# Kernel optimization log

Hardware: AMD Instinct MI355X
Metric: run time of the kernel (lower is better)

The kernel has to match this reference:

```python
import jax, jax.numpy as jnp
import numpy as np

TABLE_NUM = 16
TABLE_SIZE_LOG2 = 12
T = 1 << TABLE_SIZE_LOG2          # 4096 entries per table
FEAT = 2                          # features per entry (mini_linear in = table_num*2)
Z_DIM = 512
RES_MIN = 16
RES_MAX = 256
IMG = 256
MLP_HIDDEN = 64
OUT_DIM = 3
BATCH = 8
PRIME_Y = np.uint32(2654435761)   # instant-NGP spatial hash prime


def setup_inputs() -> dict:
    key = jax.random.key(0)
    ks = jax.random.split(key, 9)
    d_tab = TABLE_NUM * T * FEAT
    return {
        "z": jax.random.normal(ks[0], (BATCH, Z_DIM), jnp.float32),
        "w_table": jax.random.normal(ks[1], (Z_DIM, d_tab), jnp.float32) * 1e-2,
        "b_table": jnp.zeros((d_tab,), jnp.float32),
        "w1": jax.random.normal(ks[2], (TABLE_NUM * FEAT, MLP_HIDDEN), jnp.float32) * (1.0 / np.sqrt(TABLE_NUM * FEAT)),
        "b1": jnp.zeros((MLP_HIDDEN,), jnp.float32),
        "w2": jax.random.normal(ks[3], (MLP_HIDDEN, MLP_HIDDEN), jnp.float32) * (1.0 / np.sqrt(MLP_HIDDEN)),
        "b2": jnp.zeros((MLP_HIDDEN,), jnp.float32),
        "w3": jax.random.normal(ks[4], (MLP_HIDDEN, OUT_DIM), jnp.float32) * (1.0 / np.sqrt(MLP_HIDDEN)),
        "b3": jnp.zeros((OUT_DIM,), jnp.float32),
    }


def _sample_coords(b):
    c = (jnp.arange(IMG, dtype=jnp.float32) + 0.5) / IMG
    xx, yy = jnp.meshgrid(c, c, indexing="ij")  # torch.meshgrid default
    coords = jnp.stack([xx, yy], axis=-1).reshape(1, -1, 2)
    return jnp.broadcast_to(coords, (b, IMG * IMG, 2))


def _hash_retrieve(tables, coords):
    """tables: B x L x T x F; coords: B x N x 2 in [0,1). Returns B x N x (L*F)."""
    B, L, _, _ = tables.shape
    growth = np.exp((np.log(RES_MAX) - np.log(RES_MIN)) / (L - 1))
    offs = jnp.array([[0, 0], [1, 0], [0, 1], [1, 1]], dtype=jnp.uint32)  # 4 corners
    bidx = jnp.arange(B)[:, None, None]
    feats = []
    for l in range(L):
        res = jnp.float32(RES_MIN * (growth ** l))
        pos = coords * res                      # B,N,2
        pos0 = jnp.floor(pos)
        frac = pos - pos0                       # B,N,2
        corner = pos0.astype(jnp.uint32)[:, :, None, :] + offs[None, None]  # B,N,4,2
        idx = (corner[..., 0] ^ (corner[..., 1] * PRIME_Y)) & jnp.uint32(T - 1)
        f = tables[:, l][bidx, idx.astype(jnp.int32)]        # B,N,4,F gather
        fx, fy = frac[..., 0], frac[..., 1]
        w = jnp.stack([(1 - fx) * (1 - fy), fx * (1 - fy),
                       (1 - fx) * fy,       fx * fy], axis=-1)  # B,N,4
        feats.append(jnp.einsum("bncf,bnc->bnf", f, w))
    return jnp.concatenate(feats, axis=-1)


def reference(z, w_table, b_table, w1, b1, w2, b2, w3, b3):
    B = z.shape[0]
    tables = (z @ w_table + b_table).reshape(B, TABLE_NUM, T, FEAT)
    coords = _sample_coords(B).astype(tables.dtype)
    feat = _hash_retrieve(tables, coords)                    # B,N,L*F
    h = jax.nn.relu(feat @ w1 + b1)
    h = jax.nn.relu(h @ w2 + b2)
    o = jnp.tanh(h @ w3 + b3)                                # B,N,3
    return o.reshape(B, IMG, IMG, OUT_DIM).transpose(0, 3, 1, 2)
```

## Files before the change

kernel.cpp:

```cpp
#include <hip/hip_runtime.h>
#include <cmath>

#define TABLE_NUM 16
#define T_SIZE    4096
#define Z_DIM     512
#define IMG       256
#define D_TAB     (TABLE_NUM * T_SIZE * 2)
#define BATCH     8
#define HID       64
#define N_PIX     (IMG * IMG)
#define PRIME_Y   2654435761u
#define KCHUNK    4
#define KLEN      (Z_DIM / KCHUNK)
#define NG4       (D_TAB / 4)

typedef _Float16 v8h  __attribute__((ext_vector_type(8)));
typedef _Float16 v2h  __attribute__((ext_vector_type(2)));
typedef float    v4f  __attribute__((ext_vector_type(4)));

struct ResArr { float r[TABLE_NUM]; };

__global__ void prep_weights(const float* __restrict__ w1, const float* __restrict__ w2,
                             const float* __restrict__ w3, const float* __restrict__ z,
                             _Float16* __restrict__ w1T, _Float16* __restrict__ w2T,
                             _Float16* __restrict__ w3T, float* __restrict__ zT)
{
    const int t0  = blockIdx.x * 256 + threadIdx.x;
    const int stp = gridDim.x * 256;
    for (int i = t0; i < HID * 32; i += stp) {
        int n = i >> 5, k = i & 31;
        w1T[i] = (_Float16)w1[k * HID + n];
    }
    for (int i = t0; i < HID * HID; i += stp) {
        int n = i >> 6, k = i & 63;
        w2T[i] = (_Float16)w2[k * HID + n];
    }
    for (int i = t0; i < 16 * HID; i += stp) {
        int n = i >> 6, k = i & 63;
        w3T[i] = (_Float16)(n < 3 ? w3[k * 3 + n] : 0.f);
    }
    for (int i = t0; i < Z_DIM * BATCH; i += stp) {
        int k = i >> 3, b = i & 7;
        zT[i] = z[b * Z_DIM + k];
    }
}

__global__ __launch_bounds__(256) void gen_partial(
    const float* __restrict__ zT, const float* __restrict__ w,
    float* __restrict__ part)
{
    const int c  = blockIdx.x >> 7;
    const int g  = (blockIdx.x & 127) * 256 + threadIdx.x;
    const int k0 = c * KLEN;
    const float4* wp = reinterpret_cast<const float4*>(w) + g;

    float4 acc[BATCH];
#pragma unroll
    for (int b = 0; b < BATCH; ++b) acc[b] = make_float4(0.f, 0.f, 0.f, 0.f);

#pragma unroll 8
    for (int kk = 0; kk < KLEN; ++kk) {
        const int k = k0 + kk;
        float4 wv = wp[(size_t)k * NG4];
        const float* zr = zT + k * BATCH;
#pragma unroll
        for (int b = 0; b < BATCH; ++b) {
            float zv = zr[b];
            acc[b].x = fmaf(zv, wv.x, acc[b].x);
            acc[b].y = fmaf(zv, wv.y, acc[b].y);
            acc[b].z = fmaf(zv, wv.z, acc[b].z);
            acc[b].w = fmaf(zv, wv.w, acc[b].w);
        }
    }

    float4* pp = reinterpret_cast<float4*>(part);
#pragma unroll
    for (int b = 0; b < BATCH; ++b)
        pp[((size_t)(c * BATCH + b) << 15) + g] = acc[b];
}

__global__ __launch_bounds__(256) void gen_reduce(
    const float* __restrict__ part, const float* __restrict__ bt,
    float* __restrict__ tabs)
{
    const int i = blockIdx.x * 256 + threadIdx.x;
    const int b = i >> 15, g = i & (NG4 - 1);
    const float4* pp = reinterpret_cast<const float4*>(part);

    float4 s = pp[((size_t)b << 15) + g];
#pragma unroll
    for (int c = 1; c < KCHUNK; ++c) {
        float4 p = pp[((size_t)(c * BATCH + b) << 15) + g];
        s.x += p.x; s.y += p.y; s.z += p.z; s.w += p.w;
    }
    float4 bv = reinterpret_cast<const float4*>(bt)[g];
    s.x += bv.x; s.y += bv.y; s.z += bv.z; s.w += bv.w;
    reinterpret_cast<float4*>(tabs)[((size_t)b << 15) + g] = s;
}

__global__ __launch_bounds__(256) void hash_mlp(
    const float* __restrict__ tabs,
    const _Float16* __restrict__ w1T, const _Float16* __restrict__ w2T,
    const _Float16* __restrict__ w3T,
    const float* __restrict__ b1, const float* __restrict__ b2,
    const float* __restrict__ b3,
    float* __restrict__ out, ResArr res)
{
    __shared__ _Float16 mbuf[4][64][72];
    const int tid  = threadIdx.x;
    const int wid  = tid >> 6;
    const int lane = tid & 63;
    const int b    = blockIdx.x & 7;
    const int tile = blockIdx.x >> 3;
    const int i0   = (tile >> 4) * 16 + wid * 4;
    const int j0   = (tile & 15) * 16;

    const int di = lane >> 4, dj = lane & 15;
    const float cx = ((float)(i0 + di) + 0.5f) * (1.0f / IMG);
    const float cy = ((float)(j0 + dj) + 0.5f) * (1.0f / IMG);
    const float2* tb2 = reinterpret_cast<const float2*>(tabs + (size_t)b * D_TAB);

#pragma unroll 4
    for (int l = 0; l < TABLE_NUM; ++l) {
        float r  = res.r[l];
        float px = cx * r, py = cy * r;
        float fx0 = floorf(px), fy0 = floorf(py);
        float fx = px - fx0, fy = py - fy0;
        unsigned x0 = (unsigned)(int)fx0, y0 = (unsigned)(int)fy0;
        unsigned hy0 = y0 * PRIME_Y, hy1 = (y0 + 1u) * PRIME_Y;
        unsigned i00 = (x0 ^ hy0) & (T_SIZE - 1);
        unsigned i10 = ((x0 + 1u) ^ hy0) & (T_SIZE - 1);
        unsigned i01 = (x0 ^ hy1) & (T_SIZE - 1);
        unsigned i11 = ((x0 + 1u) ^ hy1) & (T_SIZE - 1);
        const float2* tl = tb2 + l * T_SIZE;
        float2 f00 = tl[i00], f10 = tl[i10], f01 = tl[i01], f11 = tl[i11];
        float w00 = (1.f - fx) * (1.f - fy);
        float w10 = fx * (1.f - fy);
        float w01 = (1.f - fx) * fy;
        float w11 = fx * fy;
        float e0 = f00.x * w00 + f10.x * w10 + f01.x * w01 + f11.x * w11;
        float e1 = f00.y * w00 + f10.y * w10 + f01.y * w01 + f11.y * w11;
        v2h p; p.x = (_Float16)e0; p.y = (_Float16)e1;
        *reinterpret_cast<v2h*>(&mbuf[wid][lane][2 * l]) = p;
    }

    const int arow = lane & 15;
    const int kgrp = lane >> 4;

    v8h a1[4];
#pragma unroll
    for (int mt = 0; mt < 4; ++mt)
        a1[mt] = *reinterpret_cast<const v8h*>(&mbuf[wid][mt * 16 + arow][kgrp * 8]);

#pragma unroll
    for (int nt = 0; nt < 4; ++nt) {
        v8h bf1 = *reinterpret_cast<const v8h*>(&w1T[(nt * 16 + arow) * 32 + kgrp * 8]);
        const float bias = b1[nt * 16 + arow];
#pragma unroll
        for (int mt = 0; mt < 4; ++mt) {
            v4f c = {0.f, 0.f, 0.f, 0.f};
            c = __builtin_amdgcn_mfma_f32_16x16x32_f16(a1[mt], bf1, c, 0, 0, 0);
#pragma unroll
            for (int e = 0; e < 4; ++e)
                mbuf[wid][mt * 16 + kgrp * 4 + e][nt * 16 + arow] =
                    (_Float16)fmaxf(c[e] + bias, 0.f);
        }
    }

    v8h a2[4][2];
#pragma unroll
    for (int mt = 0; mt < 4; ++mt) {
        a2[mt][0] = *reinterpret_cast<const v8h*>(&mbuf[wid][mt * 16 + arow][kgrp * 8]);
        a2[mt][1] = *reinterpret_cast<const v8h*>(&mbuf[wid][mt * 16 + arow][32 + kgrp * 8]);
    }
#pragma unroll
    for (int nt = 0; nt < 4; ++nt) {
        v8h bf2a = *reinterpret_cast<const v8h*>(&w2T[(nt * 16 + arow) * 64 + kgrp * 8]);
        v8h bf2b = *reinterpret_cast<const v8h*>(&w2T[(nt * 16 + arow) * 64 + 32 + kgrp * 8]);
        const float bias = b2[nt * 16 + arow];
#pragma unroll
        for (int mt = 0; mt < 4; ++mt) {
            v4f c = {0.f, 0.f, 0.f, 0.f};
            c = __builtin_amdgcn_mfma_f32_16x16x32_f16(a2[mt][0], bf2a, c, 0, 0, 0);
            c = __builtin_amdgcn_mfma_f32_16x16x32_f16(a2[mt][1], bf2b, c, 0, 0, 0);
#pragma unroll
            for (int e = 0; e < 4; ++e)
                mbuf[wid][mt * 16 + kgrp * 4 + e][nt * 16 + arow] =
                    (_Float16)fmaxf(c[e] + bias, 0.f);
        }
    }

    const float bias3 = (arow < 3) ? b3[arow] : 0.f;
#pragma unroll
    for (int mt = 0; mt < 4; ++mt) {
        v8h bf3a = *reinterpret_cast<const v8h*>(&w3T[arow * 64 + kgrp * 8]);
        v8h bf3b = *reinterpret_cast<const v8h*>(&w3T[arow * 64 + 32 + kgrp * 8]);
        v8h a0  = *reinterpret_cast<const v8h*>(&mbuf[wid][mt * 16 + arow][kgrp * 8]);
        v8h a1v = *reinterpret_cast<const v8h*>(&mbuf[wid][mt * 16 + arow][32 + kgrp * 8]);
        v4f c = {0.f, 0.f, 0.f, 0.f};
        c = __builtin_amdgcn_mfma_f32_16x16x32_f16(a0,  bf3a, c, 0, 0, 0);
        c = __builtin_amdgcn_mfma_f32_16x16x32_f16(a1v, bf3b, c, 0, 0, 0);
        if (arow < 3) {
            float4 st;
            st.x = tanhf(c[0] + bias3);
            st.y = tanhf(c[1] + bias3);
            st.z = tanhf(c[2] + bias3);
            st.w = tanhf(c[3] + bias3);
            size_t idx = ((size_t)b * 3 + arow) * N_PIX
                       + (size_t)(i0 + mt) * IMG + j0 + kgrp * 4;
            *reinterpret_cast<float4*>(&out[idx]) = st;
        }
    }
}

extern "C" void kernel_launch(void* const* d_in, const int* in_sizes, int n_in,
                              void* d_out, int out_size, void* d_ws, size_t ws_size,
                              hipStream_t stream)
{
    const float* z  = (const float*)d_in[0];
    const float* wt = (const float*)d_in[1];
    const float* bt = (const float*)d_in[2];
    const float* w1 = (const float*)d_in[3];
    const float* b1 = (const float*)d_in[4];
    const float* w2 = (const float*)d_in[5];
    const float* b2 = (const float*)d_in[6];
    const float* w3 = (const float*)d_in[7];
    const float* b3 = (const float*)d_in[8];
    float* out  = (float*)d_out;

    char* ws = (char*)d_ws;
    float*     tabs = (float*)ws;
    float*     part = (float*)(ws + (4 << 20));
    _Float16*  w1T  = (_Float16*)(ws + (20 << 20));
    _Float16*  w2T  = (_Float16*)(ws + (20 << 20) + 4096);
    _Float16*  w3T  = (_Float16*)(ws + (20 << 20) + 12288);
    float*     zT   = (float*)(ws + (20 << 20) + 16384);

    ResArr ra;
    const double growth = std::exp((std::log(256.0) - std::log(16.0)) / 15.0);
    for (int l = 0; l < TABLE_NUM; ++l)
        ra.r[l] = (float)(16.0 * std::pow(growth, (double)l));

    prep_weights<<<16, 256, 0, stream>>>(w1, w2, w3, z, w1T, w2T, w3T, zT);
    gen_partial<<<KCHUNK * (NG4 / 256), 256, 0, stream>>>(zT, wt, part);
    gen_reduce<<<BATCH * NG4 / 256, 256, 0, stream>>>(part, bt, tabs);
    hash_mlp<<<BATCH * (N_PIX / 256), 256, 0, stream>>>(
        tabs, w1T, w2T, w3T, b1, b2, b3, out, ra);
}
```

Measured before the change: 90.93 us.

## Stage per-tile hash-grid corner footprints into LDS before interpolation

Each block first gathers every hash-table entry its 16x16 pixel tile can touch, for all 16 levels, into a shared-memory buffer. The per-level footprint widths are precomputed constants. After a barrier, the bilinear interpolation reads its four corners from LDS using local grid offsets instead of issuing four scattered global gathers per level per pixel. This removes redundant global or L2 gather traffic and latency. In exchange it adds about 10KB of LDS, a block-wide sync, and integer division in the staging loop. It also relies on the WCAP bounds covering the footprint under float rounding.

New measurement: 91.66 us. Within noise of the previous version (+0.8%).

```diff
diff --git a/kernel.cpp b/kernel.cpp
--- a/kernel.cpp
+++ b/kernel.cpp
@@ -20,6 +20,10 @@
 
 struct ResArr { float r[TABLE_NUM]; };
 
+__device__ constexpr int WCAP[16]  = {3,4,4,4,5,5,5,6,7,8,9,10,11,13,15,18};
+__device__ constexpr int CBASE[16] = {0,9,25,41,57,82,107,132,168,217,281,362,462,583,752,977};
+#define CTOT 1301
+
 __global__ void prep_weights(const float* __restrict__ w1, const float* __restrict__ w2,
                              const float* __restrict__ w3, const float* __restrict__ z,
                              _Float16* __restrict__ w1T, _Float16* __restrict__ w2T,
@@ -107,33 +111,56 @@
     float* __restrict__ out, ResArr res)
 {
     __shared__ _Float16 mbuf[4][64][72];
+    __shared__ float2   cstage[CTOT];
+
     const int tid  = threadIdx.x;
     const int wid  = tid >> 6;
     const int lane = tid & 63;
     const int b    = blockIdx.x & 7;
     const int tile = blockIdx.x >> 3;
-    const int i0   = (tile >> 4) * 16 + wid * 4;
-    const int j0   = (tile & 15) * 16;
+    const int i0b  = (tile >> 4) * 16;
+    const int j0b  = (tile & 15) * 16;
+    const int i0   = i0b + wid * 4;
 
     const int di = lane >> 4, dj = lane & 15;
-    const float cx = ((float)(i0 + di) + 0.5f) * (1.0f / IMG);
-    const float cy = ((float)(j0 + dj) + 0.5f) * (1.0f / IMG);
+    const float cxp = ((float)(i0 + di) + 0.5f) * (1.0f / IMG);
+    const float cyp = ((float)(j0b + dj) + 0.5f) * (1.0f / IMG);
     const float2* tb2 = reinterpret_cast<const float2*>(tabs + (size_t)b * D_TAB);
 
-#pragma unroll 4
+    const float cx_lo = ((float)i0b + 0.5f) * (1.0f / IMG);
+    const float cy_lo = ((float)j0b + 0.5f) * (1.0f / IMG);
+
+#pragma unroll
     for (int l = 0; l < TABLE_NUM; ++l) {
-        float r  = res.r[l];
-        float px = cx * r, py = cy * r;
+        const float r  = res.r[l];
+        const int   xs = (int)floorf(cx_lo * r);
+        const int   ys = (int)floorf(cy_lo * r);
+        const float2* tl = tb2 + l * T_SIZE;
+        const int W = WCAP[l], CNT = WCAP[l] * WCAP[l];
+        for (int e = tid; e < CNT; e += 256) {
+            int yy = e / W, xx = e - yy * W;
+            unsigned idx = ((unsigned)(xs + xx) ^
+                            ((unsigned)(ys + yy) * PRIME_Y)) & (T_SIZE - 1);
+            cstage[CBASE[l] + e] = tl[idx];
+        }
+    }
+    __syncthreads();
+
+#pragma unroll
+    for (int l = 0; l < TABLE_NUM; ++l) {
+        const float r   = res.r[l];
+        const float xsf = floorf(cx_lo * r);
+        const float ysf = floorf(cy_lo * r);
+        float px = cxp * r, py = cyp * r;
         float fx0 = floorf(px), fy0 = floorf(py);
         float fx = px - fx0, fy = py - fy0;
-        unsigned x0 = (unsigned)(int)fx0, y0 = (unsigned)(int)fy0;
-        unsigned hy0 = y0 * PRIME_Y, hy1 = (y0 + 1u) * PRIME_Y;
-        unsigned i00 = (x0 ^ hy0) & (T_SIZE - 1);
-        unsigned i10 = ((x0 + 1u) ^ hy0) & (T_SIZE - 1);
-        unsigned i01 = (x0 ^ hy1) & (T_SIZE - 1);
-        unsigned i11 = ((x0 + 1u) ^ hy1) & (T_SIZE - 1);
-        const float2* tl = tb2 + l * T_SIZE;
-        float2 f00 = tl[i00], f10 = tl[i10], f01 = tl[i01], f11 = tl[i11];
+        int xi = (int)(fx0 - xsf), yi = (int)(fy0 - ysf);
+        const float2* cb = cstage + CBASE[l];
+        const int W = WCAP[l];
+        float2 f00 = cb[yi * W + xi];
+        float2 f10 = cb[yi * W + xi + 1];
+        float2 f01 = cb[(yi + 1) * W + xi];
+        float2 f11 = cb[(yi + 1) * W + xi + 1];
         float w00 = (1.f - fx) * (1.f - fy);
         float w10 = fx * (1.f - fy);
         float w01 = (1.f - fx) * fy;
@@ -207,7 +234,7 @@
             st.z = tanhf(c[2] + bias3);
             st.w = tanhf(c[3] + bias3);
             size_t idx = ((size_t)b * 3 + arow) * N_PIX
-                       + (size_t)(i0 + mt) * IMG + j0 + kgrp * 4;
+                       + (size_t)(i0 + mt) * IMG + j0b + kgrp * 4;
             *reinterpret_cast<float4*>(&out[idx]) = st;
         }
     }
```

## Compute hash features directly into MFMA A-fragment registers, skipping LDS staging

Applied to the files above, without the earlier changes.

Each lane now computes the interpolated hash features for exactly the (pixel, level) pairs it needs in its MFMA A operand, four levels times four pixel rows. Previously every lane computed all 16 levels for one pixel, wrote them to shared memory and read them back in fragment layout. This removes the LDS write/read round trip and lets y-hash terms be shared across the four rows. The trade-off is a different gather access pattern and more live registers per lane.

Result: no change. 90.81 us (-0.1%).

```diff
diff --git a/kernel.cpp b/kernel.cpp
--- a/kernel.cpp
+++ b/kernel.cpp
@@ -115,42 +115,47 @@
     const int i0   = (tile >> 4) * 16 + wid * 4;
     const int j0   = (tile & 15) * 16;
 
-    const int di = lane >> 4, dj = lane & 15;
-    const float cx = ((float)(i0 + di) + 0.5f) * (1.0f / IMG);
-    const float cy = ((float)(j0 + dj) + 0.5f) * (1.0f / IMG);
-    const float2* tb2 = reinterpret_cast<const float2*>(tabs + (size_t)b * D_TAB);
-
-#pragma unroll 4
-    for (int l = 0; l < TABLE_NUM; ++l) {
-        float r  = res.r[l];
-        float px = cx * r, py = cy * r;
-        float fx0 = floorf(px), fy0 = floorf(py);
-        float fx = px - fx0, fy = py - fy0;
-        unsigned x0 = (unsigned)(int)fx0, y0 = (unsigned)(int)fy0;
-        unsigned hy0 = y0 * PRIME_Y, hy1 = (y0 + 1u) * PRIME_Y;
-        unsigned i00 = (x0 ^ hy0) & (T_SIZE - 1);
-        unsigned i10 = ((x0 + 1u) ^ hy0) & (T_SIZE - 1);
-        unsigned i01 = (x0 ^ hy1) & (T_SIZE - 1);
-        unsigned i11 = ((x0 + 1u) ^ hy1) & (T_SIZE - 1);
-        const float2* tl = tb2 + l * T_SIZE;
-        float2 f00 = tl[i00], f10 = tl[i10], f01 = tl[i01], f11 = tl[i11];
-        float w00 = (1.f - fx) * (1.f - fy);
-        float w10 = fx * (1.f - fy);
-        float w01 = (1.f - fx) * fy;
-        float w11 = fx * fy;
-        float e0 = f00.x * w00 + f10.x * w10 + f01.x * w01 + f11.x * w11;
-        float e1 = f00.y * w00 + f10.y * w10 + f01.y * w01 + f11.y * w11;
-        v2h p; p.x = (_Float16)e0; p.y = (_Float16)e1;
-        *reinterpret_cast<v2h*>(&mbuf[wid][lane][2 * l]) = p;
-    }
-
     const int arow = lane & 15;
     const int kgrp = lane >> 4;
 
+    const float2* tb2 = reinterpret_cast<const float2*>(tabs + (size_t)b * D_TAB);
+
+    const float cyp = ((float)(j0 + arow) + 0.5f) * (1.0f / IMG);
     v8h a1[4];
 #pragma unroll
-    for (int mt = 0; mt < 4; ++mt)
-        a1[mt] = *reinterpret_cast<const v8h*>(&mbuf[wid][mt * 16 + arow][kgrp * 8]);
+    for (int q = 0; q < 4; ++q) {
+        const float r = (kgrp == 0) ? res.r[q]
+                      : (kgrp == 1) ? res.r[4 + q]
+                      : (kgrp == 2) ? res.r[8 + q]
+                      :               res.r[12 + q];
+        const float2* tl = tb2 + (kgrp * 4 + q) * T_SIZE;
+        float py = cyp * r;
+        float fy0 = floorf(py);
+        float fy = py - fy0;
+        unsigned y0 = (unsigned)(int)fy0;
+        unsigned hy0 = y0 * PRIME_Y, hy1 = (y0 + 1u) * PRIME_Y;
+#pragma unroll
+        for (int mt = 0; mt < 4; ++mt) {
+            const float cxp = ((float)(i0 + mt) + 0.5f) * (1.0f / IMG);
+            float px = cxp * r;
+            float fx0 = floorf(px);
+            float fx = px - fx0;
+            unsigned x0 = (unsigned)(int)fx0;
+            unsigned i00 = (x0 ^ hy0) & (T_SIZE - 1);
+            unsigned i10 = ((x0 + 1u) ^ hy0) & (T_SIZE - 1);
+            unsigned i01 = (x0 ^ hy1) & (T_SIZE - 1);
+            unsigned i11 = ((x0 + 1u) ^ hy1) & (T_SIZE - 1);
+            float2 f00 = tl[i00], f10 = tl[i10], f01 = tl[i01], f11 = tl[i11];
+            float w00 = (1.f - fx) * (1.f - fy);
+            float w10 = fx * (1.f - fy);
+            float w01 = (1.f - fx) * fy;
+            float w11 = fx * fy;
+            float e0 = f00.x * w00 + f10.x * w10 + f01.x * w01 + f11.x * w11;
+            float e1 = f00.y * w00 + f10.y * w10 + f01.y * w01 + f11.y * w11;
+            a1[mt][2 * q]     = (_Float16)e0;
+            a1[mt][2 * q + 1] = (_Float16)e1;
+        }
+    }
 
 #pragma unroll
     for (int nt = 0; nt < 4; ++nt) {
```
